# Kernel tuning notes

Hardware: AMD Instinct MI355X
Metric: run time of the kernel (lower is better)

The kernel has to match this reference:

```python
import jax, jax.numpy as jnp
import numpy as np

N_NODES = 50000
N_EDGES = 800000
IN_C, HID_C, OUT_C = 96, 64, 40
ALPHA = 0.2
K = 2
NEG_SLOPE = 0.01  # F.leaky_relu default


def setup_inputs() -> dict:
    key = jax.random.key(0)
    k_x, k_e, k_w0, k_b0, k_w4, k_b4 = jax.random.split(key, 6)
    x = jax.random.normal(k_x, (N_NODES, IN_C), dtype=jnp.float32)
    edge_index = jax.random.randint(k_e, (2, N_EDGES), 0, N_NODES, dtype=jnp.int64)
    # SGConv linear layers (torch.nn.Linear layout: [out, in])
    W0 = jax.random.normal(k_w0, (HID_C, IN_C), dtype=jnp.float32) / np.sqrt(IN_C)
    b0 = jax.random.normal(k_b0, (HID_C,), dtype=jnp.float32) * 0.01
    W4 = jax.random.normal(k_w4, (OUT_C, HID_C), dtype=jnp.float32) / np.sqrt(HID_C)
    b4 = jax.random.normal(k_b4, (OUT_C,), dtype=jnp.float32) * 0.01
    return {"x": x, "edge_index": edge_index, "W0": W0, "b0": b0, "W4": W4, "b4": b4}


def reference(x, edge_index, W0, b0, W4, b4):
    # GCN normalization with self-loops (shared by SGConv and APPNP in PyG):
    # A_hat = A + I, prop(h) = D^{-1/2} A_hat D^{-1/2} h
    n = x.shape[0]
    loops = jnp.arange(n, dtype=edge_index.dtype)
    src = jnp.concatenate([edge_index[0], loops])
    dst = jnp.concatenate([edge_index[1], loops])
    deg = jax.ops.segment_sum(jnp.ones_like(dst, dtype=x.dtype), dst, num_segments=n)
    dinv = jnp.where(deg > 0, jax.lax.rsqrt(deg), 0.0)
    norm = dinv[src] * dinv[dst]  # [E + N]

    def prop(h):
        # gather -> scale -> scatter-add  (irregular memory-bound core op)
        return jax.ops.segment_sum(norm[:, None] * h[src], dst, num_segments=n)

    def sg_prop(h):  # SGConv: K propagation steps, then linear
        for _ in range(K):
            h = prop(h)
        return h

    def appnp(h0):  # APPNP: z_{k+1} = (1-alpha) * prop(z_k) + alpha * h0
        z = h0
        for _ in range(K):
            z = (1.0 - ALPHA) * prop(z) + ALPHA * h0
        return z

    h = sg_prop(x) @ W0.T + b0          # conv0 (SGConv)
    # dropout is identity in eval mode (training=False)
    h = jax.nn.leaky_relu(appnp(h), NEG_SLOPE)   # conv1
    h = jax.nn.leaky_relu(appnp(h), NEG_SLOPE)   # conv2
    h = jax.nn.leaky_relu(appnp(h), NEG_SLOPE)   # conv3
    h = sg_prop(h) @ W4.T + b4          # conv4 (SGConv)
    return jax.nn.log_softmax(h, axis=1)
```

## Files before the change

### kernel.cpp

```cpp
#include <hip/hip_runtime.h>
#include <hip/hip_fp16.h>
#include <math.h>

#define N_NODES 50000
#define N_EDGES 800000
#define IN_C 96
#define HID_C 64
#define OUT_C 40
#define ALPHA 0.2f
#define NEG_SLOPE 0.01f
#define QCAP 131072

#define PLANE_H ((size_t)N_NODES * 32)
#define PLANE_F4 ((size_t)N_NODES * 4)

typedef _Float16 f16x8 __attribute__((ext_vector_type(8)));
typedef float f32x4 __attribute__((ext_vector_type(4)));

__device__ __forceinline__ int edge_at(const void* ei, int is64, long long pos) {
    return is64 ? (int)((const long long*)ei)[pos] : ((const int*)ei)[pos];
}

__global__ void zero_detect_k(int* deg, int n, int* qtail, const unsigned int* ei, int* flag) {
    int i = blockIdx.x * blockDim.x + threadIdx.x;
    if (i < n) deg[i] = 0;
    if (i < 8) qtail[i] = 0;
    if (i == 0) {
        int is64 = 1;
        for (int j = 1; j < 16; j += 2)
            if (ei[j] != 0u) is64 = 0;
        *flag = is64;
    }
}

__global__ void bucketA_k(const void* ei, const int* flag, int* __restrict__ deg,
                          int* __restrict__ qtail, int2* __restrict__ queue, int E) {
    __shared__ int cnt[8], qb[8];
    int f = *flag;
    int e0 = blockIdx.x * 1024;
    if (threadIdx.x < 8) cnt[threadIdx.x] = 0;
    __syncthreads();
    int s[4], d[4], p[4], r[4];
    #pragma unroll
    for (int k = 0; k < 4; ++k) {
        int e = e0 + threadIdx.x + k * 256;
        if (e < E) {
            d[k] = edge_at(ei, f, (long long)E + e);
            s[k] = edge_at(ei, f, e);
            atomicAdd(&deg[d[k]], 1);
            p[k] = d[k] / (N_NODES / 8);
            if (p[k] > 7) p[k] = 7;
            r[k] = atomicAdd(&cnt[p[k]], 1);
        } else p[k] = -1;
    }
    __syncthreads();
    if (threadIdx.x < 8) qb[threadIdx.x] = atomicAdd(&qtail[threadIdx.x], cnt[threadIdx.x]);
    __syncthreads();
    #pragma unroll
    for (int k = 0; k < 4; ++k) {
        if (p[k] >= 0) {
            int pos = qb[p[k]] + r[k];
            if (pos < QCAP) queue[(size_t)p[k] * QCAP + pos] = make_int2(s[k], d[k]);
        }
    }
}

__global__ void bucketB_k(const int* __restrict__ qtail, const int2* __restrict__ queue,
                          int* __restrict__ cursor, int* __restrict__ csrc) {
    int p = blockIdx.x & 7;
    int j = blockIdx.x >> 3;
    int J = gridDim.x >> 3;
    int n = qtail[p]; if (n > QCAP) n = QCAP;
    const int2* q = queue + (size_t)p * QCAP;
    for (int i = j * blockDim.x + threadIdx.x; i < n; i += J * blockDim.x) {
        int2 e = q[i];
        int pos = atomicAdd(&cursor[e.y], 1);
        csrc[pos] = e.x;
    }
}

__global__ void scan_p1_k(const int* __restrict__ deg, int* __restrict__ part, int n) {
    __shared__ int sm[256];
    int t = threadIdx.x, i = blockIdx.x * 256 + t;
    int v = (i < n) ? deg[i] : 0;
    sm[t] = v;
    __syncthreads();
    for (int off = 1; off < 256; off <<= 1) {
        int u = (t >= off) ? sm[t - off] : 0;
        __syncthreads();
        sm[t] += u;
        __syncthreads();
    }
    if (t == 255) part[blockIdx.x] = sm[255];
}

__global__ void scan_p2_k(int* part, int nb, int* rowptr, int n) {
    __shared__ int sm[256];
    int t = threadIdx.x;
    int v = (t < nb) ? part[t] : 0;
    sm[t] = v;
    __syncthreads();
    for (int off = 1; off < 256; off <<= 1) {
        int u = (t >= off) ? sm[t - off] : 0;
        __syncthreads();
        sm[t] += u;
        __syncthreads();
    }
    if (t < nb) part[t] = sm[t] - v;
    if (t == 255) rowptr[n] = sm[255];
}

__global__ void scan_p3_k(const int* __restrict__ deg, const int* __restrict__ part,
                          int* __restrict__ rowptr, int* __restrict__ cursor,
                          float* __restrict__ dinv, int* __restrict__ bcnt, int n) {
    __shared__ int sm[256];
    __shared__ int h[64];
    int t = threadIdx.x, i = blockIdx.x * 256 + t;
    if (t < 64) h[t] = 0;
    int v = (i < n) ? deg[i] : 0;
    sm[t] = v;
    __syncthreads();
    for (int off = 1; off < 256; off <<= 1) {
        int u = (t >= off) ? sm[t - off] : 0;
        __syncthreads();
        sm[t] += u;
        __syncthreads();
    }
    if (i < n) {
        int excl = sm[t] - v + part[blockIdx.x];
        rowptr[i] = excl;
        cursor[i] = excl;
        dinv[i] = rsqrtf((float)v + 1.0f);
        int dd = v; if (dd > 63) dd = 63;
        atomicAdd(&h[63 - dd], 1);
    }
    __syncthreads();
    if (t < 64) bcnt[blockIdx.x * 64 + t] = h[t];
}

__global__ void bscanA_k(const int* __restrict__ bcnt, int* __restrict__ bbase,
                         int* __restrict__ tot, int nb) {
    __shared__ int sm[256];
    int b = blockIdx.x;
    int t = threadIdx.x;
    int v = (t < nb) ? bcnt[t * 64 + b] : 0;
    sm[t] = v;
    __syncthreads();
    for (int off = 1; off < 256; off <<= 1) {
        int u = (t >= off) ? sm[t - off] : 0;
        __syncthreads();
        sm[t] += u;
        __syncthreads();
    }
    if (t < nb) bbase[t * 64 + b] = sm[t] - v;
    if (t == 255) tot[b] = sm[255];
}

__global__ void perm_k(const int* __restrict__ deg, const int* __restrict__ bbase,
                       const int* __restrict__ tot, int* __restrict__ perm, int n) {
    __shared__ int h[64], bs[64];
    int t = threadIdx.x, i = blockIdx.x * 256 + t;
    if (t < 64) { h[t] = 0; bs[t] = tot[t]; }
    __syncthreads();
    if (t == 0) {
        int run = 0;
        for (int k = 0; k < 64; ++k) { int v = bs[k]; bs[k] = run; run += v; }
    }
    __syncthreads();
    if (i < n) {
        int d = deg[i]; if (d > 63) d = 63;
        int b = 63 - d;
        int rank = atomicAdd(&h[b], 1);
        perm[bs[b] + bbase[blockIdx.x * 64 + b] + rank] = i;
    }
}

__device__ __forceinline__ void add8(float* acc, float4 v, float w) {
    const __half2* hp = (const __half2*)&v;
    #pragma unroll
    for (int j = 0; j < 4; ++j) {
        float2 f = __half22float2(hp[j]);
        acc[2 * j] += w * f.x;
        acc[2 * j + 1] += w * f.y;
    }
}

template <bool COMBINE, bool LEAKY, bool BIAS>
__global__ void __launch_bounds__(256) prop32_k(
        const int* __restrict__ perm,
        const int* __restrict__ rowptr, const int* __restrict__ csrc,
        const float* __restrict__ dinv,
        const __half* __restrict__ in, const __half* __restrict__ h0,
        const float* __restrict__ bias,
        __half* __restrict__ out, int N) {
    int half = blockIdx.x & 1;
    int g = (blockIdx.x >> 1) * (blockDim.x >> 2) + (threadIdx.x >> 2);
    int ci = threadIdx.x & 3;
    if (g >= N) return;
    int node = perm[g];
    const float4* in4 = (const float4*)in + (size_t)half * PLANE_F4;
    float acc[8];
    {
        float4 r = in4[(size_t)node * 4 + ci];
        const __half2* hp = (const __half2*)&r;
        #pragma unroll
        for (int j = 0; j < 4; ++j) {
            float2 f = __half22float2(hp[j]);
            acc[2 * j] = f.x;
            acc[2 * j + 1] = f.y;
        }
    }
    int r0 = rowptr[node], r1 = rowptr[node + 1];
    int i = r0;
    for (; i + 3 < r1; i += 4) {
        int s0 = csrc[i], s1 = csrc[i + 1], s2 = csrc[i + 2], s3 = csrc[i + 3];
        float4 v0 = in4[(size_t)s0 * 4 + ci];
        float4 v1 = in4[(size_t)s1 * 4 + ci];
        float4 v2 = in4[(size_t)s2 * 4 + ci];
        float4 v3 = in4[(size_t)s3 * 4 + ci];
        add8(acc, v0, 1.0f);
        add8(acc, v1, 1.0f);
        add8(acc, v2, 1.0f);
        add8(acc, v3, 1.0f);
    }
    for (; i < r1; ++i) {
        float4 v0 = in4[(size_t)csrc[i] * 4 + ci];
        add8(acc, v0, 1.0f);
    }
    float di = dinv[node];
    float sc = di * di;
    float v[8];
    #pragma unroll
    for (int j = 0; j < 8; ++j) v[j] = sc * acc[j];
    if (BIAS) {
        float4 b0v = ((const float4*)bias)[half * 8 + 2 * ci];
        float4 b1v = ((const float4*)bias)[half * 8 + 2 * ci + 1];
        v[0] += di * b0v.x; v[1] += di * b0v.y; v[2] += di * b0v.z; v[3] += di * b0v.w;
        v[4] += di * b1v.x; v[5] += di * b1v.y; v[6] += di * b1v.z; v[7] += di * b1v.w;
    }
    if (COMBINE) {
        float4 r = ((const float4*)h0 + (size_t)half * PLANE_F4)[(size_t)node * 4 + ci];
        const __half2* hp = (const __half2*)&r;
        #pragma unroll
        for (int j = 0; j < 4; ++j) {
            float2 f = __half22float2(hp[j]);
            v[2 * j]     = (1.0f - ALPHA) * v[2 * j]     + ALPHA * f.x;
            v[2 * j + 1] = (1.0f - ALPHA) * v[2 * j + 1] + ALPHA * f.y;
        }
    }
    if (LEAKY) {
        #pragma unroll
        for (int j = 0; j < 8; ++j) v[j] = v[j] > 0.0f ? v[j] : NEG_SLOPE * v[j];
    }
    float4 o;
    __half2* op = (__half2*)&o;
    #pragma unroll
    for (int j = 0; j < 4; ++j)
        op[j] = __float22half2_rn(make_float2(v[2 * j], v[2 * j + 1]));
    ((float4*)out + (size_t)half * PLANE_F4)[(size_t)node * 4 + ci] = o;
}

__global__ void __launch_bounds__(256) prop40_k(
        const int* __restrict__ perm,
        const int* __restrict__ rowptr, const int* __restrict__ csrc,
        const float* __restrict__ dinv,
        const __half* __restrict__ in, __half* __restrict__ out, int N) {
    int g = blockIdx.x * (blockDim.x >> 3) + (threadIdx.x >> 3);
    int ci = threadIdx.x & 7;
    if (g >= N) return;
    int node = perm[g];
    bool act = ci < 5;
    const float4* in4 = (const float4*)in;
    float acc[8] = {0.f, 0.f, 0.f, 0.f, 0.f, 0.f, 0.f, 0.f};
    if (act) {
        float4 r = in4[(size_t)node * 5 + ci];
        const __half2* hp = (const __half2*)&r;
        #pragma unroll
        for (int j = 0; j < 4; ++j) {
            float2 f = __half22float2(hp[j]);
            acc[2 * j] = f.x;
            acc[2 * j + 1] = f.y;
        }
    }
    int r0 = rowptr[node], r1 = rowptr[node + 1];
    int i = r0;
    for (; i + 3 < r1; i += 4) {
        int s0 = csrc[i], s1 = csrc[i + 1], s2 = csrc[i + 2], s3 = csrc[i + 3];
        if (act) {
            float4 v0 = in4[(size_t)s0 * 5 + ci];
            float4 v1 = in4[(size_t)s1 * 5 + ci];
            float4 v2 = in4[(size_t)s2 * 5 + ci];
            float4 v3 = in4[(size_t)s3 * 5 + ci];
            add8(acc, v0, 1.0f);
            add8(acc, v1, 1.0f);
            add8(acc, v2, 1.0f);
            add8(acc, v3, 1.0f);
        }
    }
    for (; i < r1; ++i) {
        int s0 = csrc[i];
        if (act) {
            float4 v0 = in4[(size_t)s0 * 5 + ci];
            add8(acc, v0, 1.0f);
        }
    }
    if (act) {
        float di = dinv[node];
        float sc = di * di;
        float4 o;
        __half2* op = (__half2*)&o;
        #pragma unroll
        for (int j = 0; j < 4; ++j)
            op[j] = __float22half2_rn(make_float2(sc * acc[2 * j], sc * acc[2 * j + 1]));
        ((float4*)out)[(size_t)node * 5 + ci] = o;
    }
}

__global__ void __launch_bounds__(256) prop40_softmax_k(
        const int* __restrict__ perm,
        const int* __restrict__ rowptr, const int* __restrict__ csrc,
        const float* __restrict__ dinv,
        const __half* __restrict__ in, const float* __restrict__ bias,
        float* __restrict__ out, int N) {
    int g = blockIdx.x * (blockDim.x >> 3) + (threadIdx.x >> 3);
    int ci = threadIdx.x & 7;
    if (g >= N) return;
    int node = perm[g];
    bool act = ci < 5;
    const float4* in4 = (const float4*)in;
    float acc[8] = {0.f, 0.f, 0.f, 0.f, 0.f, 0.f, 0.f, 0.f};
    if (act) {
        float4 r = in4[(size_t)node * 5 + ci];
        const __half2* hp = (const __half2*)&r;
        #pragma unroll
        for (int j = 0; j < 4; ++j) {
            float2 f = __half22float2(hp[j]);
            acc[2 * j] = f.x;
            acc[2 * j + 1] = f.y;
        }
    }
    int r0 = rowptr[node], r1 = rowptr[node + 1];
    int i = r0;
    for (; i + 3 < r1; i += 4) {
        int s0 = csrc[i], s1 = csrc[i + 1], s2 = csrc[i + 2], s3 = csrc[i + 3];
        if (act) {
            float4 v0 = in4[(size_t)s0 * 5 + ci];
            float4 v1 = in4[(size_t)s1 * 5 + ci];
            float4 v2 = in4[(size_t)s2 * 5 + ci];
            float4 v3 = in4[(size_t)s3 * 5 + ci];
            add8(acc, v0, 1.0f);
            add8(acc, v1, 1.0f);
            add8(acc, v2, 1.0f);
            add8(acc, v3, 1.0f);
        }
    }
    for (; i < r1; ++i) {
        int s0 = csrc[i];
        if (act) {
            float4 v0 = in4[(size_t)s0 * 5 + ci];
            add8(acc, v0, 1.0f);
        }
    }
    float di = dinv[node];
    float v[8];
    if (act) {
        float4 b0v = ((const float4*)bias)[2 * ci];
        float4 b1v = ((const float4*)bias)[2 * ci + 1];
        v[0] = di * acc[0] + b0v.x; v[1] = di * acc[1] + b0v.y;
        v[2] = di * acc[2] + b0v.z; v[3] = di * acc[3] + b0v.w;
        v[4] = di * acc[4] + b1v.x; v[5] = di * acc[5] + b1v.y;
        v[6] = di * acc[6] + b1v.z; v[7] = di * acc[7] + b1v.w;
    } else {
        #pragma unroll
        for (int j = 0; j < 8; ++j) v[j] = -INFINITY;
    }
    float m = v[0];
    #pragma unroll
    for (int j = 1; j < 8; ++j) m = fmaxf(m, v[j]);
    #pragma unroll
    for (int off = 4; off >= 1; off >>= 1) m = fmaxf(m, __shfl_xor(m, off));
    float e = 0.0f;
    if (act) {
        #pragma unroll
        for (int j = 0; j < 8; ++j) e += expf(v[j] - m);
    }
    #pragma unroll
    for (int off = 4; off >= 1; off >>= 1) e += __shfl_xor(e, off);
    float ls = m + logf(e);
    if (act) {
        float4 o0 = make_float4(v[0] - ls, v[1] - ls, v[2] - ls, v[3] - ls);
        float4 o1 = make_float4(v[4] - ls, v[5] - ls, v[6] - ls, v[7] - ls);
        ((float4*)out)[(size_t)node * 10 + 2 * ci] = o0;
        ((float4*)out)[(size_t)node * 10 + 2 * ci + 1] = o1;
    }
}

template <int O, int K, bool FP32IN, bool SCALE, bool PIN, bool POUT>
__global__ void __launch_bounds__(256) mfma_lin_k(const void* __restrict__ in_,
                                                  const float* __restrict__ W,
                                                  const float* __restrict__ dinv,
                                                  __half* __restrict__ out, int Mtiles) {
    constexpr int P2 = 52;
    __shared__ __half2 wsh[O * P2];
    for (int idx = threadIdx.x; idx < O * (K / 2); idx += 256) {
        int o = idx / (K / 2), kk = idx - o * (K / 2);
        float2 w2 = ((const float2*)W)[o * (K / 2) + kk];
        wsh[o * P2 + kk] = __floats2half2_rn(w2.x, w2.y);
    }
    __syncthreads();
    int wave = (blockIdx.x * 256 + threadIdx.x) >> 6;
    if (wave >= Mtiles) return;
    int lane = threadIdx.x & 63;
    int lm = lane & 15, q = lane >> 4;
    long long m0 = (long long)wave * 16;
    constexpr int NT = (O + 15) / 16;
    f32x4 acc[NT];
    #pragma unroll
    for (int j = 0; j < NT; ++j) acc[j] = (f32x4){0.f, 0.f, 0.f, 0.f};
    const __half* wsp = (const __half*)wsh;
    #pragma unroll
    for (int k0 = 0; k0 < K; k0 += 32) {
        f16x8 a;
        if (FP32IN) {
            const float* xr = (const float*)in_ + (m0 + lm) * K + k0 + q * 8;
            float4 x0 = ((const float4*)xr)[0];
            float4 x1 = ((const float4*)xr)[1];
            a = (f16x8){(_Float16)x0.x, (_Float16)x0.y, (_Float16)x0.z, (_Float16)x0.w,
                        (_Float16)x1.x, (_Float16)x1.y, (_Float16)x1.z, (_Float16)x1.w};
        } else if (PIN) {
            const __half* xr = (const __half*)in_ + (size_t)(k0 >> 5) * PLANE_H
                               + (m0 + lm) * 32 + q * 8;
            a = *(const f16x8*)xr;
        } else {
            const __half* xr = (const __half*)in_ + (m0 + lm) * K + k0 + q * 8;
            a = *(const f16x8*)xr;
        }
        #pragma unroll
        for (int j = 0; j < NT; ++j) {
            f16x8 b = *(const f16x8*)(wsp + (16 * j + lm) * (2 * P2) + k0 + q * 8);
            acc[j] = __builtin_amdgcn_mfma_f32_16x16x32_f16(a, b, acc[j], 0, 0, 0);
        }
    }
    #pragma unroll
    for (int r = 0; r < 4; ++r) {
        long long m = m0 + q * 4 + r;
        float sc = SCALE ? dinv[m] : 1.0f;
        #pragma unroll
        for (int j = 0; j < NT; ++j) {
            int col = 16 * j + lm;
            if (POUT) {
                out[(size_t)(col >> 5) * PLANE_H + m * 32 + (col & 31)] =
                    __float2half(acc[j][r] * sc);
            } else if (col < O) {
                out[m * O + col] = __float2half(acc[j][r] * sc);
            }
        }
    }
}

static inline int cdiv(long long a, long long b) { return (int)((a + b - 1) / b); }
static inline size_t align256(size_t x) { return (x + 255) & ~(size_t)255; }

extern "C" void kernel_launch(void* const* d_in, const int* in_sizes, int n_in,
                              void* d_out, int out_size, void* d_ws, size_t ws_size,
                              hipStream_t stream) {
    const float* x  = (const float*)d_in[0];
    const void*  ei = d_in[1];
    const float* W0 = (const float*)d_in[2];
    const float* b0 = (const float*)d_in[3];
    const float* W4 = (const float*)d_in[4];
    const float* b4 = (const float*)d_in[5];
    float* out = (float*)d_out;

    const int N = N_NODES, E = N_EDGES;
    const int NB = cdiv(N, 256);
    char* ws = (char*)d_ws;
    int*    flag   = (int*)ws;     ws += 256;
    int*    deg    = (int*)ws;     ws += align256((size_t)N * 4);
    int*    rowptr = (int*)ws;     ws += align256((size_t)(N + 1) * 4);
    int*    cursor = (int*)ws;     ws += align256((size_t)N * 4);
    int*    part   = (int*)ws;     ws += align256(256 * 4);
    int*    bcnt   = (int*)ws;     ws += align256((size_t)NB * 64 * 4);
    int*    bbase  = (int*)ws;     ws += align256((size_t)NB * 64 * 4);
    int*    tot    = (int*)ws;     ws += align256(64 * 4);
    int*    qtail  = (int*)ws;     ws += align256(8 * 4);
    int*    perm   = (int*)ws;     ws += align256((size_t)N * 4);
    float*  dinv   = (float*)ws;   ws += align256((size_t)N * 4);
    int*    csrc   = (int*)ws;     ws += align256((size_t)E * 4);
    int2*   queue  = (int2*)ws;    ws += align256((size_t)8 * QCAP * 8);
    __half* bufA   = (__half*)ws;  ws += align256((size_t)N * HID_C * 2);
    __half* bufB   = (__half*)ws;  ws += align256((size_t)N * HID_C * 2);
    __half* bufC   = (__half*)ws;  ws += align256((size_t)N * HID_C * 2);

    const int T = 256;
    const int MT = N / 16;
    const int LB = cdiv(MT, 4);
    const int P32B = 2 * cdiv(N, T / 4);
    const int P40B = cdiv(N, T / 8);

    zero_detect_k<<<cdiv(N, T), T, 0, stream>>>(deg, N, qtail, (const unsigned int*)ei, flag);
    bucketA_k<<<cdiv(E, 1024), T, 0, stream>>>(ei, flag, deg, qtail, queue, E);
    scan_p1_k<<<NB, 256, 0, stream>>>(deg, part, N);
    scan_p2_k<<<1, 256, 0, stream>>>(part, NB, rowptr, N);
    scan_p3_k<<<NB, 256, 0, stream>>>(deg, part, rowptr, cursor, dinv, bcnt, N);
    bscanA_k<<<64, 256, 0, stream>>>(bcnt, bbase, tot, NB);
    perm_k<<<NB, 256, 0, stream>>>(deg, bbase, tot, perm, N);
    bucketB_k<<<8 * 64, T, 0, stream>>>(qtail, queue, cursor, csrc);

    mfma_lin_k<HID_C, IN_C, true, true, false, true><<<LB, 256, 0, stream>>>(
        x, W0, dinv, bufA, MT);
    prop32_k<false, false, false><<<P32B, T, 0, stream>>>(
        perm, rowptr, csrc, dinv, bufA, nullptr, nullptr, bufB, N);
    prop32_k<false, false, true><<<P32B, T, 0, stream>>>(
        perm, rowptr, csrc, dinv, bufB, nullptr, b0, bufC, N);

    for (int r = 0; r < 3; ++r) {
        prop32_k<true, false, false><<<P32B, T, 0, stream>>>(
            perm, rowptr, csrc, dinv, bufC, bufC, nullptr, bufB, N);
        prop32_k<true, true, false><<<P32B, T, 0, stream>>>(
            perm, rowptr, csrc, dinv, bufB, bufC, nullptr, bufC, N);
    }

    mfma_lin_k<OUT_C, HID_C, false, false, true, false><<<LB, 256, 0, stream>>>(
        bufC, W4, dinv, bufA, MT);
    prop40_k<<<P40B, T, 0, stream>>>(perm, rowptr, csrc, dinv, bufA, bufB, N);
    prop40_softmax_k<<<P40B, T, 0, stream>>>(perm, rowptr, csrc, dinv, bufB, b4, out, N);
}
```

Measured before the change: 368.3 us.

## Switch feature buffers from split 32-channel planes to contiguous 64-wide rows with 8-wide gather

```diff
diff --git a/kernel.cpp b/kernel.cpp
--- a/kernel.cpp
+++ b/kernel.cpp
@@ -10,9 +10,6 @@
 #define ALPHA 0.2f
 #define NEG_SLOPE 0.01f
 #define QCAP 131072
-
-#define PLANE_H ((size_t)N_NODES * 32)
-#define PLANE_F4 ((size_t)N_NODES * 4)
 
 typedef _Float16 f16x8 __attribute__((ext_vector_type(8)));
 typedef float f32x4 __attribute__((ext_vector_type(4)));
@@ -186,22 +183,21 @@
 }
 
 template <bool COMBINE, bool LEAKY, bool BIAS>
-__global__ void __launch_bounds__(256) prop32_k(
+__global__ void __launch_bounds__(256) prop64_k(
         const int* __restrict__ perm,
         const int* __restrict__ rowptr, const int* __restrict__ csrc,
         const float* __restrict__ dinv,
         const __half* __restrict__ in, const __half* __restrict__ h0,
         const float* __restrict__ bias,
         __half* __restrict__ out, int N) {
-    int half = blockIdx.x & 1;
-    int g = (blockIdx.x >> 1) * (blockDim.x >> 2) + (threadIdx.x >> 2);
-    int ci = threadIdx.x & 3;
+    int g = blockIdx.x * (blockDim.x >> 3) + (threadIdx.x >> 3);
+    int ci = threadIdx.x & 7;
     if (g >= N) return;
     int node = perm[g];
-    const float4* in4 = (const float4*)in + (size_t)half * PLANE_F4;
+    const float4* in8 = (const float4*)in;
     float acc[8];
     {
-        float4 r = in4[(size_t)node * 4 + ci];
+        float4 r = in8[node * 8 + ci];
         const __half2* hp = (const __half2*)&r;
         #pragma unroll
         for (int j = 0; j < 4; ++j) {
@@ -212,19 +208,41 @@
     }
     int r0 = rowptr[node], r1 = rowptr[node + 1];
     int i = r0;
+    int s[8];
+    if (i + 7 < r1) {
+        #pragma unroll
+        for (int j = 0; j < 8; ++j) s[j] = csrc[i + j];
+    }
+    for (; i + 15 < r1; i += 8) {
+        float4 v[8];
+        #pragma unroll
+        for (int j = 0; j < 8; ++j) v[j] = in8[(size_t)s[j] * 8 + ci];
+        #pragma unroll
+        for (int j = 0; j < 8; ++j) s[j] = csrc[i + 8 + j];
+        #pragma unroll
+        for (int j = 0; j < 8; ++j) add8(acc, v[j], 1.0f);
+    }
+    if (i + 7 < r1) {
+        float4 v[8];
+        #pragma unroll
+        for (int j = 0; j < 8; ++j) v[j] = in8[(size_t)s[j] * 8 + ci];
+        #pragma unroll
+        for (int j = 0; j < 8; ++j) add8(acc, v[j], 1.0f);
+        i += 8;
+    }
     for (; i + 3 < r1; i += 4) {
         int s0 = csrc[i], s1 = csrc[i + 1], s2 = csrc[i + 2], s3 = csrc[i + 3];
-        float4 v0 = in4[(size_t)s0 * 4 + ci];
-        float4 v1 = in4[(size_t)s1 * 4 + ci];
-        float4 v2 = in4[(size_t)s2 * 4 + ci];
-        float4 v3 = in4[(size_t)s3 * 4 + ci];
+        float4 v0 = in8[(size_t)s0 * 8 + ci];
+        float4 v1 = in8[(size_t)s1 * 8 + ci];
+        float4 v2 = in8[(size_t)s2 * 8 + ci];
+        float4 v3 = in8[(size_t)s3 * 8 + ci];
         add8(acc, v0, 1.0f);
         add8(acc, v1, 1.0f);
         add8(acc, v2, 1.0f);
         add8(acc, v3, 1.0f);
     }
     for (; i < r1; ++i) {
-        float4 v0 = in4[(size_t)csrc[i] * 4 + ci];
+        float4 v0 = in8[(size_t)csrc[i] * 8 + ci];
         add8(acc, v0, 1.0f);
     }
     float di = dinv[node];
@@ -233,13 +251,13 @@
     #pragma unroll
     for (int j = 0; j < 8; ++j) v[j] = sc * acc[j];
     if (BIAS) {
-        float4 b0v = ((const float4*)bias)[half * 8 + 2 * ci];
-        float4 b1v = ((const float4*)bias)[half * 8 + 2 * ci + 1];
+        float4 b0v = ((const float4*)bias)[2 * ci];
+        float4 b1v = ((const float4*)bias)[2 * ci + 1];
         v[0] += di * b0v.x; v[1] += di * b0v.y; v[2] += di * b0v.z; v[3] += di * b0v.w;
         v[4] += di * b1v.x; v[5] += di * b1v.y; v[6] += di * b1v.z; v[7] += di * b1v.w;
     }
     if (COMBINE) {
-        float4 r = ((const float4*)h0 + (size_t)half * PLANE_F4)[(size_t)node * 4 + ci];
+        float4 r = ((const float4*)h0)[node * 8 + ci];
         const __half2* hp = (const __half2*)&r;
         #pragma unroll
         for (int j = 0; j < 4; ++j) {
@@ -257,7 +275,7 @@
     #pragma unroll
     for (int j = 0; j < 4; ++j)
         op[j] = __float22half2_rn(make_float2(v[2 * j], v[2 * j + 1]));
-    ((float4*)out + (size_t)half * PLANE_F4)[(size_t)node * 4 + ci] = o;
+    ((float4*)out)[node * 8 + ci] = o;
 }
 
 __global__ void __launch_bounds__(256) prop40_k(
@@ -270,10 +288,11 @@
     if (g >= N) return;
     int node = perm[g];
     bool act = ci < 5;
+    int cc = act ? ci : 0;
     const float4* in4 = (const float4*)in;
-    float acc[8] = {0.f, 0.f, 0.f, 0.f, 0.f, 0.f, 0.f, 0.f};
-    if (act) {
-        float4 r = in4[(size_t)node * 5 + ci];
+    float acc[8];
+    {
+        float4 r = in4[(size_t)node * 8 + cc];
         const __half2* hp = (const __half2*)&r;
         #pragma unroll
         for (int j = 0; j < 4; ++j) {
@@ -284,25 +303,42 @@
     }
     int r0 = rowptr[node], r1 = rowptr[node + 1];
     int i = r0;
+    int s[8];
+    if (i + 7 < r1) {
+        #pragma unroll
+        for (int j = 0; j < 8; ++j) s[j] = csrc[i + j];
+    }
+    for (; i + 15 < r1; i += 8) {
+        float4 v[8];
+        #pragma unroll
+        for (int j = 0; j < 8; ++j) v[j] = in4[(size_t)s[j] * 8 + cc];
+        #pragma unroll
+        for (int j = 0; j < 8; ++j) s[j] = csrc[i + 8 + j];
+        #pragma unroll
+        for (int j = 0; j < 8; ++j) add8(acc, v[j], 1.0f);
+    }
+    if (i + 7 < r1) {
+        float4 v[8];
+        #pragma unroll
+        for (int j = 0; j < 8; ++j) v[j] = in4[(size_t)s[j] * 8 + cc];
+        #pragma unroll
+        for (int j = 0; j < 8; ++j) add8(acc, v[j], 1.0f);
+        i += 8;
+    }
     for (; i + 3 < r1; i += 4) {
         int s0 = csrc[i], s1 = csrc[i + 1], s2 = csrc[i + 2], s3 = csrc[i + 3];
-        if (act) {
-            float4 v0 = in4[(size_t)s0 * 5 + ci];
-            float4 v1 = in4[(size_t)s1 * 5 + ci];
-            float4 v2 = in4[(size_t)s2 * 5 + ci];
-            float4 v3 = in4[(size_t)s3 * 5 + ci];
-            add8(acc, v0, 1.0f);
-            add8(acc, v1, 1.0f);
-            add8(acc, v2, 1.0f);
-            add8(acc, v3, 1.0f);
-        }
+        float4 v0 = in4[(size_t)s0 * 8 + cc];
+        float4 v1 = in4[(size_t)s1 * 8 + cc];
+        float4 v2 = in4[(size_t)s2 * 8 + cc];
+        float4 v3 = in4[(size_t)s3 * 8 + cc];
+        add8(acc, v0, 1.0f);
+        add8(acc, v1, 1.0f);
+        add8(acc, v2, 1.0f);
+        add8(acc, v3, 1.0f);
     }
     for (; i < r1; ++i) {
-        int s0 = csrc[i];
-        if (act) {
-            float4 v0 = in4[(size_t)s0 * 5 + ci];
-            add8(acc, v0, 1.0f);
-        }
+        float4 v0 = in4[(size_t)csrc[i] * 8 + cc];
+        add8(acc, v0, 1.0f);
     }
     if (act) {
         float di = dinv[node];
@@ -312,7 +348,7 @@
         #pragma unroll
         for (int j = 0; j < 4; ++j)
             op[j] = __float22half2_rn(make_float2(sc * acc[2 * j], sc * acc[2 * j + 1]));
-        ((float4*)out)[(size_t)node * 5 + ci] = o;
+        ((float4*)out)[(size_t)node * 8 + ci] = o;
     }
 }
 
@@ -327,10 +363,11 @@
     if (g >= N) return;
     int node = perm[g];
     bool act = ci < 5;
+    int cc = act ? ci : 0;
     const float4* in4 = (const float4*)in;
-    float acc[8] = {0.f, 0.f, 0.f, 0.f, 0.f, 0.f, 0.f, 0.f};
-    if (act) {
-        float4 r = in4[(size_t)node * 5 + ci];
+    float acc[8];
+    {
+        float4 r = in4[(size_t)node * 8 + cc];
         const __half2* hp = (const __half2*)&r;
         #pragma unroll
         for (int j = 0; j < 4; ++j) {
@@ -341,25 +378,42 @@
     }
     int r0 = rowptr[node], r1 = rowptr[node + 1];
     int i = r0;
+    int s[8];
+    if (i + 7 < r1) {
+        #pragma unroll
+        for (int j = 0; j < 8; ++j) s[j] = csrc[i + j];
+    }
+    for (; i + 15 < r1; i += 8) {
+        float4 v[8];
+        #pragma unroll
+        for (int j = 0; j < 8; ++j) v[j] = in4[(size_t)s[j] * 8 + cc];
+        #pragma unroll
+        for (int j = 0; j < 8; ++j) s[j] = csrc[i + 8 + j];
+        #pragma unroll
+        for (int j = 0; j < 8; ++j) add8(acc, v[j], 1.0f);
+    }
+    if (i + 7 < r1) {
+        float4 v[8];
+        #pragma unroll
+        for (int j = 0; j < 8; ++j) v[j] = in4[(size_t)s[j] * 8 + cc];
+        #pragma unroll
+        for (int j = 0; j < 8; ++j) add8(acc, v[j], 1.0f);
+        i += 8;
+    }
     for (; i + 3 < r1; i += 4) {
         int s0 = csrc[i], s1 = csrc[i + 1], s2 = csrc[i + 2], s3 = csrc[i + 3];
-        if (act) {
-            float4 v0 = in4[(size_t)s0 * 5 + ci];
-            float4 v1 = in4[(size_t)s1 * 5 + ci];
-            float4 v2 = in4[(size_t)s2 * 5 + ci];
-            float4 v3 = in4[(size_t)s3 * 5 + ci];
-            add8(acc, v0, 1.0f);
-            add8(acc, v1, 1.0f);
-            add8(acc, v2, 1.0f);
-            add8(acc, v3, 1.0f);
-        }
+        float4 v0 = in4[(size_t)s0 * 8 + cc];
+        float4 v1 = in4[(size_t)s1 * 8 + cc];
+        float4 v2 = in4[(size_t)s2 * 8 + cc];
+        float4 v3 = in4[(size_t)s3 * 8 + cc];
+        add8(acc, v0, 1.0f);
+        add8(acc, v1, 1.0f);
+        add8(acc, v2, 1.0f);
+        add8(acc, v3, 1.0f);
     }
     for (; i < r1; ++i) {
-        int s0 = csrc[i];
-        if (act) {
-            float4 v0 = in4[(size_t)s0 * 5 + ci];
-            add8(acc, v0, 1.0f);
-        }
+        float4 v0 = in4[(size_t)csrc[i] * 8 + cc];
+        add8(acc, v0, 1.0f);
     }
     float di = dinv[node];
     float v[8];
@@ -395,7 +449,7 @@
     }
 }
 
-template <int O, int K, bool FP32IN, bool SCALE, bool PIN, bool POUT>
+template <int O, int K, int OP, bool FP32IN, bool SCALE>
 __global__ void __launch_bounds__(256) mfma_lin_k(const void* __restrict__ in_,
                                                   const float* __restrict__ W,
                                                   const float* __restrict__ dinv,
@@ -427,10 +481,6 @@
             float4 x1 = ((const float4*)xr)[1];
             a = (f16x8){(_Float16)x0.x, (_Float16)x0.y, (_Float16)x0.z, (_Float16)x0.w,
                         (_Float16)x1.x, (_Float16)x1.y, (_Float16)x1.z, (_Float16)x1.w};
-        } else if (PIN) {
-            const __half* xr = (const __half*)in_ + (size_t)(k0 >> 5) * PLANE_H
-                               + (m0 + lm) * 32 + q * 8;
-            a = *(const f16x8*)xr;
         } else {
             const __half* xr = (const __half*)in_ + (m0 + lm) * K + k0 + q * 8;
             a = *(const f16x8*)xr;
@@ -448,12 +498,7 @@
         #pragma unroll
         for (int j = 0; j < NT; ++j) {
             int col = 16 * j + lm;
-            if (POUT) {
-                out[(size_t)(col >> 5) * PLANE_H + m * 32 + (col & 31)] =
-                    __float2half(acc[j][r] * sc);
-            } else if (col < O) {
-                out[m * O + col] = __float2half(acc[j][r] * sc);
-            }
+            if (col < OP) out[m * OP + col] = __float2half(acc[j][r] * sc);
         }
     }
 }
@@ -495,7 +540,7 @@
     const int T = 256;
     const int MT = N / 16;
     const int LB = cdiv(MT, 4);
-    const int P32B = 2 * cdiv(N, T / 4);
+    const int P64B = cdiv(N, T / 8);
     const int P40B = cdiv(N, T / 8);
 
     zero_detect_k<<<cdiv(N, T), T, 0, stream>>>(deg, N, qtail, (const unsigned int*)ei, flag);
@@ -507,21 +552,20 @@
     perm_k<<<NB, 256, 0, stream>>>(deg, bbase, tot, perm, N);
     bucketB_k<<<8 * 64, T, 0, stream>>>(qtail, queue, cursor, csrc);
 
-    mfma_lin_k<HID_C, IN_C, true, true, false, true><<<LB, 256, 0, stream>>>(
-        x, W0, dinv, bufA, MT);
-    prop32_k<false, false, false><<<P32B, T, 0, stream>>>(
+    mfma_lin_k<HID_C, IN_C, HID_C, true, true><<<LB, 256, 0, stream>>>(x, W0, dinv, bufA, MT);
+    prop64_k<false, false, false><<<P64B, T, 0, stream>>>(
         perm, rowptr, csrc, dinv, bufA, nullptr, nullptr, bufB, N);
-    prop32_k<false, false, true><<<P32B, T, 0, stream>>>(
+    prop64_k<false, false, true><<<P64B, T, 0, stream>>>(
         perm, rowptr, csrc, dinv, bufB, nullptr, b0, bufC, N);
 
     for (int r = 0; r < 3; ++r) {
-        prop32_k<true, false, false><<<P32B, T, 0, stream>>>(
+        prop64_k<true, false, false><<<P64B, T, 0, stream>>>(
             perm, rowptr, csrc, dinv, bufC, bufC, nullptr, bufB, N);
-        prop32_k<true, true, false><<<P32B, T, 0, stream>>>(
+        prop64_k<true, true, false><<<P64B, T, 0, stream>>>(
             perm, rowptr, csrc, dinv, bufB, bufC, nullptr, bufC, N);
     }
 
-    mfma_lin_k<OUT_C, HID_C, false, false, true, false><<<LB, 256, 0, stream>>>(
+    mfma_lin_k<OUT_C, HID_C, HID_C, false, false><<<LB, 256, 0, stream>>>(
         bufC, W4, dinv, bufA, MT);
     prop40_k<<<P40B, T, 0, stream>>>(perm, rowptr, csrc, dinv, bufA, bufB, N);
     prop40_softmax_k<<<P40B, T, 0, stream>>>(perm, rowptr, csrc, dinv, bufB, b4, out, N);
```

Measured after the change: 333.9 us. -9.3%, faster.
